# Kernel tuning notes

Hardware: AMD Instinct MI355X
Metric: run time of the kernel (lower is better)

Reference implementation:

```python
import jax, jax.numpy as jnp
import numpy as np

B, S, I, C, P = 64, 14, 32, 10, 4   # batch, spatial, in-caps/pos, classes, pose size
ROUTINGS = 3
EPS = 1e-9


def setup_inputs() -> dict:
    key = jax.random.key(0)
    k1, k2, k3, k4, k5 = jax.random.split(key, 5)
    return {
        "inputs_pose": jax.random.normal(k1, (B, S, S, I, P, P), jnp.float32),
        "inputs_activation": jax.random.uniform(k2, (B, S, S, I), jnp.float32),
        "w": jax.random.normal(k3, (1, I, C, P, P), jnp.float32),
        "beta_v": jax.random.normal(k4, (1, C), jnp.float32) * 0.1,
        "beta_a": jax.random.normal(k5, (1, C), jnp.float32) * 0.1,
    }


def _em_routing(votes, i_act, beta_v, beta_a, routings):
    # votes: [B, N, C, 16], i_act: [B, N]
    Bn, N, Cc, D = votes.shape
    rr = jnp.full((Bn, N, Cc, 1), 1.0 / Cc, votes.dtype)  # uniform init assignments
    bv = beta_v.reshape(1, 1, Cc, 1)
    ba = beta_a.reshape(1, 1, Cc, 1)
    it_min, it_max = 1.0, min(float(routings), 3.0)  # inverse-temperature schedule
    o_mean = o_act = None
    for it in range(routings):
        inv_temp = it_min + (it_max - it_min) * it / max(1.0, routings - 1.0)
        # --- M step ---
        rr_p = rr * i_act[:, :, None, None]                        # [B,N,C,1]
        rr_sum = jnp.sum(rr_p, axis=1, keepdims=True)              # [B,1,C,1]
        o_mean = jnp.sum(rr_p * votes, axis=1, keepdims=True) / rr_sum   # [B,1,C,16]
        o_var = jnp.sum(rr_p * jnp.square(votes - o_mean), axis=1, keepdims=True) / rr_sum
        o_stdv = jnp.sqrt(o_var)                                   # [B,1,C,16]
        cost = jnp.sum((bv + jnp.log(o_stdv + EPS)) * rr_sum, axis=-1, keepdims=True)  # [B,1,C,1]
        o_act = jax.nn.sigmoid(inv_temp * (ba - cost))             # [B,1,C,1]
        # --- E step (skipped on last iteration) ---
        if it < routings - 1:
            logp = (-jnp.sum(jnp.square(votes - o_mean) / (2.0 * jnp.square(o_stdv) + EPS),
                             axis=-1, keepdims=True)
                    - jnp.sum(jnp.log(o_stdv + EPS), axis=-1, keepdims=True))  # [B,N,C,1]
            zz = jnp.log(o_act + EPS) + logp
            rr = jax.nn.softmax(zz, axis=2)
    return o_mean[:, 0], o_act[:, 0, :, 0]  # [B,C,16], [B,C]


def reference(inputs_pose, inputs_activation, w, beta_v, beta_a):
    # mat_transform: votes[b,h,w,i,c] = pose[b,h,w,i] @ W[i,c]   (4x4 matmuls)
    votes = jnp.einsum('bhwipq,icqr->bhwicpr', inputs_pose, w[0])
    votes = votes.reshape(B, S, S, I, C, P * P)
    # coordinate addition: scaled (row+0.5)/S onto pose element 0, col onto element 1
    coord = (jnp.arange(S, dtype=votes.dtype) + 0.5) / S
    votes = votes.at[..., 0].add(coord[None, :, None, None, None])
    votes = votes.at[..., 1].add(coord[None, None, :, None, None])
    votes = votes.reshape(B, S * S * I, C, P * P)
    acts = inputs_activation.reshape(B, S * S * I)
    o_mean, o_act = _em_routing(votes, acts, beta_v, beta_a, ROUTINGS)
    pose = o_mean.reshape(B, C, P, P)
    return pose, o_act
```

## Files before the change

kernel.cpp:

```cpp
#include <hip/hip_runtime.h>
#include <math.h>

#define Bsz 64
#define Ssz 14
#define Isz 32
#define Csz 10
#define Dsz 16
#define Nsz (Ssz*Ssz*Isz)
#define EPSF 1e-9f

#define CH   448
#define NCH  14
#define BLK  640
#define ITER (CH/64)
#define NCOPY 8

__device__ __forceinline__ void vote_reg(const float* p, const float* Wr,
                                         float chh, float cww, float* v)
{
#pragma unroll
    for (int pr = 0; pr < 4; ++pr)
#pragma unroll
        for (int r = 0; r < 4; ++r)
            v[pr*4+r] = p[pr*4+0]*Wr[0*4+r] + p[pr*4+1]*Wr[1*4+r]
                      + p[pr*4+2]*Wr[2*4+r] + p[pr*4+3]*Wr[3*4+r];
    v[0] += chh;
    v[1] += cww;
}

__device__ __forceinline__ void load_W_regs(const float* __restrict__ w,
                                            int lane, int c, float* Wr)
{
    const float4* ws = reinterpret_cast<const float4*>(w + (((lane & 31)*Csz + c) * Dsz));
    float4 b0 = ws[0], b1 = ws[1], b2 = ws[2], b3 = ws[3];
    Wr[0]=b0.x; Wr[1]=b0.y; Wr[2]=b0.z; Wr[3]=b0.w;
    Wr[4]=b1.x; Wr[5]=b1.y; Wr[6]=b1.z; Wr[7]=b1.w;
    Wr[8]=b2.x; Wr[9]=b2.y; Wr[10]=b2.z; Wr[11]=b2.w;
    Wr[12]=b3.x; Wr[13]=b3.y; Wr[14]=b3.z; Wr[15]=b3.w;
}

__device__ __forceinline__ void stage_pose(const float* __restrict__ poseb,
                                           int base, int tid, float* Pl)
{
    const float4* gp = reinterpret_cast<const float4*>(poseb + (size_t)base * Dsz);
    float4* lp = reinterpret_cast<float4*>(Pl);
    for (int f = tid; f < CH*4; f += BLK)
        lp[(f & 3)*CH + (f >> 2)] = gp[f];
}

__device__ __forceinline__ void load_pose_lds(const float* Pl, int nl, float* p)
{
    const float4* q = reinterpret_cast<const float4*>(Pl);
    float4 a0 = q[0*CH + nl], a1 = q[1*CH + nl], a2 = q[2*CH + nl], a3 = q[3*CH + nl];
    p[0]=a0.x; p[1]=a0.y; p[2]=a0.z; p[3]=a0.w;
    p[4]=a1.x; p[5]=a1.y; p[6]=a1.z; p[7]=a1.w;
    p[8]=a2.x; p[9]=a2.y; p[10]=a2.z; p[11]=a2.w;
    p[12]=a3.x; p[13]=a3.y; p[14]=a3.z; p[15]=a3.w;
}

__device__ __forceinline__ void reduce_store(float s0, float* s1, float* s2,
                                             float* __restrict__ pt, int lane)
{
#pragma unroll
    for (int m = 1; m <= 4; m <<= 1) {
        s0 += __shfl_xor(s0, m);
#pragma unroll
        for (int d = 0; d < Dsz; ++d) {
            s1[d] += __shfl_xor(s1[d], m);
            s2[d] += __shfl_xor(s2[d], m);
        }
    }
    if ((lane & 7) == 0) {
        float* po = pt + (lane >> 3) * 33;
        po[0] = s0;
#pragma unroll
        for (int d = 0; d < Dsz; ++d) { po[1+d] = s1[d]; po[17+d] = s2[d]; }
    }
}

__global__ __launch_bounds__(BLK) void m0_kernel(
    const float* __restrict__ pose,
    const float* __restrict__ act,
    const float* __restrict__ w,
    float* __restrict__ partials)
{
    const int b = blockIdx.x, chunk = blockIdx.y;
    const int tid = threadIdx.x, c = tid >> 6, lane = tid & 63;
    const int base = chunk * CH;

    __shared__ float Pl[4*CH*4];

    const float* poseb = pose + (size_t)b * Nsz * Dsz;
    stage_pose(poseb, base, tid, Pl);

    float Wr[16];
    load_W_regs(w, lane, c, Wr);
    __syncthreads();

    float s0 = 0.f, s1[Dsz], s2[Dsz];
#pragma unroll
    for (int d = 0; d < Dsz; ++d) { s1[d] = 0.f; s2[d] = 0.f; }

    const float* actb = act + (size_t)b * Nsz;

    for (int it = 0; it < ITER; ++it) {
        const int nl = it*64 + lane;
        const int n  = base + nl;
        float p[16];
        load_pose_lds(Pl, nl, p);
        int hw = n >> 5;
        int wc = hw % Ssz, hr = hw / Ssz;
        float wgt = actb[n] * (1.0f/Csz);
        float v[16];
        vote_reg(p, Wr, (hr+0.5f)*(1.0f/Ssz), (wc+0.5f)*(1.0f/Ssz), v);
        s0 += wgt;
#pragma unroll
        for (int d = 0; d < Dsz; ++d) {
            float wv = wgt * v[d];
            s1[d] += wv;
            s2[d] += wv * v[d];
        }
    }

    float* pt = partials + ((size_t)((b*Csz + c)*NCH + chunk))*NCOPY*33;
    reduce_store(s0, s1, s2, pt, lane);
}

__global__ __launch_bounds__(BLK) void em_kernel(
    const float* __restrict__ pose,
    const float* __restrict__ act,
    const float* __restrict__ w,
    const float* __restrict__ beta_v,
    const float* __restrict__ beta_a,
    const float* __restrict__ part_in,
    float* __restrict__ part_out,
    float inv_temp_prev)
{
    const int b = blockIdx.x, chunk = blockIdx.y;
    const int tid = threadIdx.x, wv = tid >> 6, lane = tid & 63;
    const int base = chunk * CH;

    __shared__ float Pl[4*CH*4];
    __shared__ float zz[CH][11];
    __shared__ float Sv[Csz][33];
    __shared__ float prm[Csz][33];
    __shared__ float lg[Csz][16];

    const float* poseb = pose + (size_t)b * Nsz * Dsz;
    stage_pose(poseb, base, tid, Pl);

    float Wr[16];
    load_W_regs(w, lane, wv, Wr);

    if (tid < Csz*33) {
        int c = tid / 33, j = tid - c*33;
        const float* pp = part_in + ((size_t)(b*Csz + c)*NCH)*NCOPY*33 + j;
        float s = 0.f;
        for (int t = 0; t < NCH*NCOPY; ++t) s += pp[t*33];
        Sv[c][j] = s;
    }
    __syncthreads();
    if (tid < Csz*Dsz) {
        int c = tid >> 4, d = tid & 15;
        float S0 = Sv[c][0];
        float mn  = Sv[c][1+d] / S0;
        float var = fmaxf(Sv[c][17+d] / S0 - mn*mn, 0.f);
        prm[c][d]    = mn;
        prm[c][16+d] = 1.f / (2.f*var + EPSF);
        lg[c][d]     = __logf(sqrtf(var) + EPSF);
    }
    __syncthreads();
    if (tid < Csz) {
        int c = tid;
        float sumlog = 0.f;
#pragma unroll
        for (int d = 0; d < Dsz; ++d) sumlog += lg[c][d];
        float cost = Sv[c][0] * (16.f * beta_v[c] + sumlog);
        float oact = 1.f / (1.f + __expf(-inv_temp_prev * (beta_a[c] - cost)));
        prm[c][32] = __logf(oact + EPSF) - sumlog;
    }
    __syncthreads();

    {
        float mn[Dsz], iv[Dsz];
#pragma unroll
        for (int d = 0; d < Dsz; ++d) { mn[d] = prm[wv][d]; iv[d] = prm[wv][16+d]; }
        float Kc = prm[wv][32];

        for (int it = 0; it < ITER; ++it) {
            const int nl = it*64 + lane;
            const int n  = base + nl;
            float p[16];
            load_pose_lds(Pl, nl, p);
            int hw = n >> 5;
            int wc = hw % Ssz, hr = hw / Ssz;
            float v[16];
            vote_reg(p, Wr, (hr+0.5f)*(1.0f/Ssz), (wc+0.5f)*(1.0f/Ssz), v);
            float qa = 0.f, qb = 0.f, qc = 0.f, qd = 0.f;
#pragma unroll
            for (int d = 0; d < 4; ++d) {
                float d0 = v[d]    - mn[d];    qa += d0*d0*iv[d];
                float d1 = v[4+d]  - mn[4+d];  qb += d1*d1*iv[4+d];
                float d2 = v[8+d]  - mn[8+d];  qc += d2*d2*iv[8+d];
                float d3 = v[12+d] - mn[12+d]; qd += d3*d3*iv[12+d];
            }
            zz[nl][wv] = Kc - ((qa+qb)+(qc+qd));
        }
    }
    __syncthreads();

    if (tid < CH) {
        const int n = base + tid;
        float z[Csz];
#pragma unroll
        for (int c = 0; c < Csz; ++c) z[c] = zz[tid][c];
        float zmax = z[0];
#pragma unroll
        for (int c = 1; c < Csz; ++c) zmax = fmaxf(zmax, z[c]);
        float zsum = 0.f;
#pragma unroll
        for (int c = 0; c < Csz; ++c) { z[c] = __expf(z[c] - zmax); zsum += z[c]; }
        float sc = __fdividef(act[(size_t)b*Nsz + n], zsum);
#pragma unroll
        for (int c = 0; c < Csz; ++c) zz[tid][c] = z[c] * sc;
    }
    __syncthreads();

    float s0 = 0.f, s1[Dsz], s2[Dsz];
#pragma unroll
    for (int d = 0; d < Dsz; ++d) { s1[d] = 0.f; s2[d] = 0.f; }

    for (int it = 0; it < ITER; ++it) {
        const int nl = it*64 + lane;
        const int n  = base + nl;
        float p[16];
        load_pose_lds(Pl, nl, p);
        int hw = n >> 5;
        int wc = hw % Ssz, hr = hw / Ssz;
        float wgt = zz[nl][wv];
        float v[16];
        vote_reg(p, Wr, (hr+0.5f)*(1.0f/Ssz), (wc+0.5f)*(1.0f/Ssz), v);
        s0 += wgt;
#pragma unroll
        for (int d = 0; d < Dsz; ++d) {
            float wvv = wgt * v[d];
            s1[d] += wvv;
            s2[d] += wvv * v[d];
        }
    }

    float* pt = part_out + ((size_t)((b*Csz + wv)*NCH + chunk))*NCOPY*33;
    reduce_store(s0, s1, s2, pt, lane);
}

__global__ __launch_bounds__(64) void fin_kernel(
    const float* __restrict__ partials,
    const float* __restrict__ beta_v,
    const float* __restrict__ beta_a,
    float* __restrict__ out,
    float inv_temp)
{
    const int bc = blockIdx.x;
    const int c = bc % Csz;
    const int tid = threadIdx.x;

    __shared__ float S[33];
    __shared__ float lgs[16];

    if (tid < 33) {
        const float* pp = partials + (size_t)bc * NCH * NCOPY * 33 + tid;
        float s = 0.f;
        for (int t = 0; t < NCH*NCOPY; ++t) s += pp[t*33];
        S[tid] = s;
    }
    __syncthreads();
    if (tid < Dsz) {
        float S0 = S[0];
        float mn  = S[1+tid] / S0;
        float var = fmaxf(S[17+tid] / S0 - mn*mn, 0.f);
        lgs[tid] = __logf(sqrtf(var) + EPSF);
        out[(size_t)bc * Dsz + tid] = mn;
    }
    __syncthreads();
    if (tid == 0) {
        float sumlog = 0.f;
#pragma unroll
        for (int d = 0; d < Dsz; ++d) sumlog += lgs[d];
        float cost = S[0] * (16.f * beta_v[c] + sumlog);
        float oact = 1.f / (1.f + __expf(-inv_temp * (beta_a[c] - cost)));
        out[Bsz*Csz*Dsz + bc] = oact;
    }
}

extern "C" void kernel_launch(void* const* d_in, const int* in_sizes, int n_in,
                              void* d_out, int out_size, void* d_ws, size_t ws_size,
                              hipStream_t stream)
{
    const float* pose = (const float*)d_in[0];
    const float* act  = (const float*)d_in[1];
    const float* w    = (const float*)d_in[2];
    const float* bv   = (const float*)d_in[3];
    const float* ba   = (const float*)d_in[4];
    float* out = (float*)d_out;

    float* partA = (float*)d_ws;
    float* partB = partA + (size_t)Bsz*Csz*NCH*NCOPY*33;

    dim3 grid(Bsz, NCH);

    m0_kernel<<<grid, BLK, 0, stream>>>(pose, act, w, partA);
    em_kernel<<<grid, BLK, 0, stream>>>(pose, act, w, bv, ba, partA, partB, 1.0f);
    em_kernel<<<grid, BLK, 0, stream>>>(pose, act, w, bv, ba, partB, partA, 2.0f);
    fin_kernel<<<Bsz*Csz, 64, 0, stream>>>(partA, bv, ba, out, 3.0f);
}
```

Baseline: 237.6 us.

## Fuse E-step softmax into M-step loop and fully reduce partials per wavefront

The E-step logp computation, the per-point softmax and the weighted M-step accumulation are merged into a single loop over 64-point slabs. Each slab uses a double-buffered shared-memory exchange of logits and one barrier per iteration. This drops the separate second vote recomputation pass, the full-chunk zz buffer and the extra barriers. The wavefront reduction now covers all 64 lanes, so each chunk writes one partial instead of eight, which shrinks the cross-chunk sums in later kernels. Coordinate indices are updated incrementally instead of with per-iteration divides, and activations are staged in LDS. The cost is a barrier inside the loop and a longer shuffle reduction.

```diff
diff --git a/kernel.cpp b/kernel.cpp
--- a/kernel.cpp
+++ b/kernel.cpp
@@ -13,7 +13,6 @@
 #define NCH  14
 #define BLK  640
 #define ITER (CH/64)
-#define NCOPY 8
 
 __device__ __forceinline__ void vote_reg(const float* p, const float* Wr,
                                          float chh, float cww, float* v)
@@ -62,7 +61,7 @@
                                              float* __restrict__ pt, int lane)
 {
 #pragma unroll
-    for (int m = 1; m <= 4; m <<= 1) {
+    for (int m = 32; m >= 1; m >>= 1) {
         s0 += __shfl_xor(s0, m);
 #pragma unroll
         for (int d = 0; d < Dsz; ++d) {
@@ -70,11 +69,10 @@
             s2[d] += __shfl_xor(s2[d], m);
         }
     }
-    if ((lane & 7) == 0) {
-        float* po = pt + (lane >> 3) * 33;
-        po[0] = s0;
-#pragma unroll
-        for (int d = 0; d < Dsz; ++d) { po[1+d] = s1[d]; po[17+d] = s2[d]; }
+    if (lane == 0) {
+        pt[0] = s0;
+#pragma unroll
+        for (int d = 0; d < Dsz; ++d) { pt[1+d] = s1[d]; pt[17+d] = s2[d]; }
     }
 }
 
@@ -103,14 +101,14 @@
 
     const float* actb = act + (size_t)b * Nsz;
 
+    int hw = (base + lane) >> 5;
+    int hr = hw / Ssz, wc = hw - hr * Ssz;
+
     for (int it = 0; it < ITER; ++it) {
         const int nl = it*64 + lane;
-        const int n  = base + nl;
         float p[16];
         load_pose_lds(Pl, nl, p);
-        int hw = n >> 5;
-        int wc = hw % Ssz, hr = hw / Ssz;
-        float wgt = actb[n] * (1.0f/Csz);
+        float wgt = actb[base + nl] * (1.0f/Csz);
         float v[16];
         vote_reg(p, Wr, (hr+0.5f)*(1.0f/Ssz), (wc+0.5f)*(1.0f/Ssz), v);
         s0 += wgt;
@@ -120,9 +118,11 @@
             s1[d] += wv;
             s2[d] += wv * v[d];
         }
-    }
-
-    float* pt = partials + ((size_t)((b*Csz + c)*NCH + chunk))*NCOPY*33;
+        wc += 2;
+        if (wc >= Ssz) { wc -= Ssz; hr += 1; }
+    }
+
+    float* pt = partials + ((size_t)((b*Csz + c)*NCH + chunk))*33;
     reduce_store(s0, s1, s2, pt, lane);
 }
 
@@ -141,22 +141,25 @@
     const int base = chunk * CH;
 
     __shared__ float Pl[4*CH*4];
-    __shared__ float zz[CH][11];
+    __shared__ float zbuf[2][64][11];
+    __shared__ float av[CH];
     __shared__ float Sv[Csz][33];
     __shared__ float prm[Csz][33];
     __shared__ float lg[Csz][16];
 
     const float* poseb = pose + (size_t)b * Nsz * Dsz;
     stage_pose(poseb, base, tid, Pl);
+    if (tid < CH) av[tid] = act[(size_t)b*Nsz + base + tid];
 
     float Wr[16];
     load_W_regs(w, lane, wv, Wr);
 
     if (tid < Csz*33) {
         int c = tid / 33, j = tid - c*33;
-        const float* pp = part_in + ((size_t)(b*Csz + c)*NCH)*NCOPY*33 + j;
+        const float* pp = part_in + ((size_t)(b*Csz + c)*NCH)*33 + j;
         float s = 0.f;
-        for (int t = 0; t < NCH*NCOPY; ++t) s += pp[t*33];
+#pragma unroll
+        for (int ch2 = 0; ch2 < NCH; ++ch2) s += pp[ch2*33];
         Sv[c][j] = s;
     }
     __syncthreads();
@@ -181,75 +184,61 @@
     }
     __syncthreads();
 
-    {
-        float mn[Dsz], iv[Dsz];
-#pragma unroll
-        for (int d = 0; d < Dsz; ++d) { mn[d] = prm[wv][d]; iv[d] = prm[wv][16+d]; }
-        float Kc = prm[wv][32];
-
-        for (int it = 0; it < ITER; ++it) {
-            const int nl = it*64 + lane;
-            const int n  = base + nl;
-            float p[16];
-            load_pose_lds(Pl, nl, p);
-            int hw = n >> 5;
-            int wc = hw % Ssz, hr = hw / Ssz;
-            float v[16];
-            vote_reg(p, Wr, (hr+0.5f)*(1.0f/Ssz), (wc+0.5f)*(1.0f/Ssz), v);
-            float qa = 0.f, qb = 0.f, qc = 0.f, qd = 0.f;
-#pragma unroll
-            for (int d = 0; d < 4; ++d) {
-                float d0 = v[d]    - mn[d];    qa += d0*d0*iv[d];
-                float d1 = v[4+d]  - mn[4+d];  qb += d1*d1*iv[4+d];
-                float d2 = v[8+d]  - mn[8+d];  qc += d2*d2*iv[8+d];
-                float d3 = v[12+d] - mn[12+d]; qd += d3*d3*iv[12+d];
-            }
-            zz[nl][wv] = Kc - ((qa+qb)+(qc+qd));
+    float mn[Dsz], iv[Dsz];
+#pragma unroll
+    for (int d = 0; d < Dsz; ++d) { mn[d] = prm[wv][d]; iv[d] = prm[wv][16+d]; }
+    const float Kc = prm[wv][32];
+
+    float s0 = 0.f, s1[Dsz], s2[Dsz];
+#pragma unroll
+    for (int d = 0; d < Dsz; ++d) { s1[d] = 0.f; s2[d] = 0.f; }
+
+    int hw = (base + lane) >> 5;
+    int hr = hw / Ssz, wc = hw - hr * Ssz;
+
+    for (int it = 0; it < ITER; ++it) {
+        const int nl = it*64 + lane;
+        float p[16];
+        load_pose_lds(Pl, nl, p);
+        float v[16];
+        vote_reg(p, Wr, (hr+0.5f)*(1.0f/Ssz), (wc+0.5f)*(1.0f/Ssz), v);
+
+        float qa = 0.f, qb = 0.f, qc = 0.f, qd = 0.f;
+#pragma unroll
+        for (int d = 0; d < 4; ++d) {
+            float d0 = v[d]    - mn[d];    qa += d0*d0*iv[d];
+            float d1 = v[4+d]  - mn[4+d];  qb += d1*d1*iv[4+d];
+            float d2 = v[8+d]  - mn[8+d];  qc += d2*d2*iv[8+d];
+            float d3 = v[12+d] - mn[12+d]; qd += d3*d3*iv[12+d];
         }
-    }
-    __syncthreads();
-
-    if (tid < CH) {
-        const int n = base + tid;
+        const int buf = it & 1;
+        zbuf[buf][lane][wv] = Kc - ((qa+qb)+(qc+qd));
+        __syncthreads();
+
         float z[Csz];
 #pragma unroll
-        for (int c = 0; c < Csz; ++c) z[c] = zz[tid][c];
+        for (int c = 0; c < Csz; ++c) z[c] = zbuf[buf][lane][c];
         float zmax = z[0];
 #pragma unroll
         for (int c = 1; c < Csz; ++c) zmax = fmaxf(zmax, z[c]);
         float zsum = 0.f;
 #pragma unroll
         for (int c = 0; c < Csz; ++c) { z[c] = __expf(z[c] - zmax); zsum += z[c]; }
-        float sc = __fdividef(act[(size_t)b*Nsz + n], zsum);
-#pragma unroll
-        for (int c = 0; c < Csz; ++c) zz[tid][c] = z[c] * sc;
-    }
-    __syncthreads();
-
-    float s0 = 0.f, s1[Dsz], s2[Dsz];
-#pragma unroll
-    for (int d = 0; d < Dsz; ++d) { s1[d] = 0.f; s2[d] = 0.f; }
-
-    for (int it = 0; it < ITER; ++it) {
-        const int nl = it*64 + lane;
-        const int n  = base + nl;
-        float p[16];
-        load_pose_lds(Pl, nl, p);
-        int hw = n >> 5;
-        int wc = hw % Ssz, hr = hw / Ssz;
-        float wgt = zz[nl][wv];
-        float v[16];
-        vote_reg(p, Wr, (hr+0.5f)*(1.0f/Ssz), (wc+0.5f)*(1.0f/Ssz), v);
-        s0 += wgt;
+        float rr = z[wv] * __fdividef(av[nl], zsum);
+
+        s0 += rr;
 #pragma unroll
         for (int d = 0; d < Dsz; ++d) {
-            float wvv = wgt * v[d];
+            float wvv = rr * v[d];
             s1[d] += wvv;
             s2[d] += wvv * v[d];
         }
-    }
-
-    float* pt = part_out + ((size_t)((b*Csz + wv)*NCH + chunk))*NCOPY*33;
+
+        wc += 2;
+        if (wc >= Ssz) { wc -= Ssz; hr += 1; }
+    }
+
+    float* pt = part_out + ((size_t)((b*Csz + wv)*NCH + chunk))*33;
     reduce_store(s0, s1, s2, pt, lane);
 }
 
@@ -268,9 +257,10 @@
     __shared__ float lgs[16];
 
     if (tid < 33) {
-        const float* pp = partials + (size_t)bc * NCH * NCOPY * 33 + tid;
+        const float* pp = partials + (size_t)bc * NCH * 33 + tid;
         float s = 0.f;
-        for (int t = 0; t < NCH*NCOPY; ++t) s += pp[t*33];
+#pragma unroll
+        for (int t = 0; t < NCH; ++t) s += pp[t*33];
         S[tid] = s;
     }
     __syncthreads();
@@ -304,7 +294,7 @@
     float* out = (float*)d_out;
 
     float* partA = (float*)d_ws;
-    float* partB = partA + (size_t)Bsz*Csz*NCH*NCOPY*33;
+    float* partB = partA + (size_t)Bsz*Csz*NCH*33;
 
     dim3 grid(Bsz, NCH);
 
```

Measured after the change: 254.4 us. 7.0% more time.
